# Optimization experiments

Hardware: AMD Instinct MI355X
Metric: run time of the kernel (lower is better)

The kernel has to match this reference:

```python
import jax, jax.numpy as jnp
import numpy as np

B, CIN, COUT = 16, 32, 64
H = W = 64
K = 3                      # kernel side
GRID_SIZE, SPLINE_ORDER = 5, 3
P = K * K                  # in_features of each KANLinear
GR0, GR1 = -1.0, 1.0       # grid_range


def make_grid():
    # torch: grid = arange(-k, G+k+1)*h + grid_range[0], expanded to (in_features, G+2k+1)
    h = (GR1 - GR0) / GRID_SIZE
    g = jnp.arange(-SPLINE_ORDER, GRID_SIZE + SPLINE_ORDER + 1, dtype=jnp.float32) * h + GR0
    return jnp.broadcast_to(g, (P, g.shape[0]))


def b_splines(x, grid):
    # Cox-de Boor recursion. x: (..., P) -> bases: (..., P, GRID_SIZE+SPLINE_ORDER)
    xe = x[..., None]
    bases = ((xe >= grid[:, :-1]) & (xe < grid[:, 1:])).astype(x.dtype)
    for j in range(1, SPLINE_ORDER + 1):
        left = (xe - grid[:, : -(j + 1)]) / (grid[:, j:-1] - grid[:, : -(j + 1)])
        right = (grid[:, j + 1 :] - xe) / (grid[:, j + 1 :] - grid[:, 1:-j])
        bases = left * bases[..., :-1] + right * bases[..., 1:]
    return bases


def setup_inputs() -> dict:
    key = jax.random.key(0)
    k1, k2, k3, k4 = jax.random.split(key, 4)
    x = jax.random.normal(k1, (B, CIN, H, W), dtype=jnp.float32)
    base_weight = jax.random.normal(k2, (COUT, CIN, P), dtype=jnp.float32) * (1.0 / np.sqrt(P))
    spline_weight = jax.random.normal(k3, (COUT, CIN, P, GRID_SIZE + SPLINE_ORDER), dtype=jnp.float32) * 0.1
    spline_scaler = jax.random.normal(k4, (COUT, CIN, P), dtype=jnp.float32) * (1.0 / np.sqrt(P))
    return {"x": x, "base_weight": base_weight, "spline_weight": spline_weight, "spline_scaler": spline_scaler}


def reference(x, base_weight, spline_weight, spline_scaler):
    grid = make_grid()
    # im2col like torch.nn.Unfold: (B, CIN*P, Hout, Wout), channel-major feature order
    patches = jax.lax.conv_general_dilated_patches(x, (K, K), (1, 1), "VALID")
    _, _, Ho, Wo = patches.shape
    patches = patches.reshape(B, CIN, P, Ho * Wo).transpose(0, 1, 3, 2)  # (B, CIN, L, P)
    # base branch: SiLU(x) @ base_weight^T, summed over input channels per output channel
    base_out = jnp.einsum("bclp,ocp->bol", jax.nn.silu(patches), base_weight)
    # spline branch: B-spline bases contracted with scaled spline weights
    bases = b_splines(patches, grid)                       # (B, CIN, L, P, G+k)
    scaled_w = spline_weight * spline_scaler[..., None]    # (COUT, CIN, P, G+k)
    spline_out = jnp.einsum("bclpg,ocpg->bol", bases, scaled_w)
    return (base_out + spline_out).reshape(B, COUT, Ho, Wo)
```

## Files before the change

kernel.cpp:

```cpp
#include <hip/hip_runtime.h>


typedef short v8s __attribute__((ext_vector_type(8)));
typedef float v4f __attribute__((ext_vector_type(4)));
typedef int   v4i __attribute__((ext_vector_type(4)));
typedef int   v8i __attribute__((ext_vector_type(8)));

#define WMX_OFF     20972032u
#define WF8_OFF     21103104u
#define WPACKS_OFF  21119488u

#define SCALE1 0x7F7F7F7Fu

__device__ __forceinline__ unsigned short f2bf(float f) {
  unsigned int u = __float_as_uint(f);
  u += 0x7fffu + ((u >> 16) & 1u);
  return (unsigned short)(u >> 16);
}

__global__ __launch_bounds__(256) void k_wpack(const float* __restrict__ bw,
                                               const float* __restrict__ sw,
                                               const float* __restrict__ sc,
                                               unsigned char* __restrict__ ws) {
  const int bid = blockIdx.x, t = threadIdx.x;
  if (bid < 72) {
    const int idx = bid * 256 + t;
    const int o = idx / 288, rem = idx - o * 288;
    const int c = rem / 9, p_tap = rem - c * 9;
    const float scv = sc[idx];
    const float4 v0 = *(const float4*)(sw + (size_t)idx * 8);
    const float4 v1 = *(const float4*)(sw + (size_t)idx * 8 + 4);
    unsigned lo = __builtin_amdgcn_cvt_pk_fp8_f32(v0.x * scv, v0.y * scv, 0, false);
    lo = __builtin_amdgcn_cvt_pk_fp8_f32(v0.z * scv, v0.w * scv, lo, true);
    unsigned hi = __builtin_amdgcn_cvt_pk_fp8_f32(v1.x * scv, v1.y * scv, 0, false);
    hi = __builtin_amdgcn_cvt_pk_fp8_f32(v1.z * scv, v1.w * scv, hi, true);
    const int di = p_tap / 3, dj = p_tap - di * 3;
    const int k0 = 24 * (c * 3 + di) + 8 * dj;
    const int p = k0 / 288, r288 = k0 - p * 288;
    const int ot = o >> 4, ol = o & 15;
    size_t dst;
    if (r288 < 256) {
      const int ss = r288 >> 7, r128 = r288 & 127;
      const int lh = r128 >> 5, r32 = r128 & 31;
      const int pc = r32 >> 4, bh = r32 & 15;
      dst = WMX_OFF + p * 16384 + ss * 8192 + ot * 2048 + pc * 1024 +
            (lh * 16 + ol) * 16 + bh;
    } else {
      const int r2 = r288 - 256;
      dst = WF8_OFF + p * 2048 + ot * 512 + ((r2 >> 3) * 16 + ol) * 8;
    }
    *(unsigned long long*)(ws + dst) =
        (unsigned long long)lo | ((unsigned long long)hi << 32);
  } else {
    const int idx2 = (bid - 72) * 256 + t;
    if (idx2 >= 2048) return;
    const int o = idx2 >> 5, cc = idx2 & 31;
    const int ot = o >> 4;
    const int lane = ((cc >> 3) << 4) | (o & 15);
    const int e = cc & 7;
#pragma unroll
    for (int sp = 0; sp < 9; ++sp) {
      const float val = bw[(size_t)(o * 32 + cc) * 9 + sp];
      *(unsigned short*)(ws + WPACKS_OFF + sp * 4096 + ot * 1024 + lane * 16 + e * 2) =
          f2bf(val);
    }
  }
}

__device__ __forceinline__ void ld16(unsigned char* ldsp, const unsigned char* gp) {
  __builtin_amdgcn_global_load_lds(
      (const __attribute__((address_space(1))) unsigned int*)gp,
      (__attribute__((address_space(3))) unsigned int*)ldsp, 16, 0, 0);
}

__global__ __launch_bounds__(512) void k_gemm(const unsigned char* __restrict__ ws,
                                              const float* __restrict__ x,
                                              float* __restrict__ out) {
  __shared__ __align__(16) unsigned char wl8[2][18432];
  __shared__ __align__(16) unsigned char fl8[2][12544];
  __shared__ __align__(16) unsigned char wsil[36864];
  __shared__ __align__(16) unsigned char fsil[25088];

  const int blk = blockIdx.x;
  const int b = blk >> 4, ig = blk & 15;
  const int i0 = ig * 4;
  const int tid = threadIdx.x;
  const int wave = tid >> 6, lane = tid & 63;
  const int q = lane >> 4, ln = lane & 15;
  const int r = wave >> 1, oh = wave & 1;
  const int i = i0 + r;

  const bool factive = tid < 384;
  const int frow = tid >> 6, fx = tid & 63;
  const int fy = min(i0 + frow, 63);

  auto stage_w = [&](int p, int bi) {
#pragma unroll
    for (int it = 0; it < 3; ++it) {
      const int u = wave + it * 8;
      if (u < 16) {
        ld16(&wl8[bi][u * 1024], ws + WMX_OFF + (size_t)p * 16384 + (size_t)u * 1024 + lane * 16);
      } else if (u < 18) {
        ld16(&wl8[bi][u * 1024], ws + WF8_OFF + (size_t)p * 2048 + (size_t)(u - 16) * 1024 + lane * 16);
      }
    }
  };

  auto stage_wsil = [&]() {
#pragma unroll
    for (int it = 0; it < 5; ++it) {
      const int u = wave + it * 8;
      if (u < 36) ld16(&wsil[u * 1024], ws + WPACKS_OFF + (size_t)u * 1024 + lane * 16);
    }
  };

  auto feat_load = [&](int p, float* v) {
    if (factive) {
#pragma unroll
      for (int cp = 0; cp < 4; ++cp)
        v[cp] = x[((size_t)(b * 32 + p * 4 + cp) * 64 + fy) * 64 + fx];
    }
  };

  auto feat_store = [&](int p, int bi, const float* v) {
    if (factive) {
      unsigned long long spl[4];
      unsigned short hh[4];
#pragma unroll
      for (int cp = 0; cp < 4; ++cp) {
        const float vv = v[cp];
        hh[cp] = f2bf(vv / (1.0f + __expf(-vv)));
        float s = (vv + 2.2f) * 2.5f;
        int ii = (int)floorf(s);
        ii = ii < 0 ? 0 : (ii > 10 ? 10 : ii);
        const float uu = (vv + 2.2f) - 0.4f * (float)ii;
        float N0 = (0.4f - uu) * 2.5f;
        float N1 = uu * 2.5f;
        float a0 = N0 * 1.25f, a1 = N1 * 1.25f;
        N0 = (0.4f - uu) * a0;
        float N2 = uu * a1;
        N1 = (uu + 0.4f) * a0 + (0.8f - uu) * a1;
        float c0 = N0 * (1.0f / 1.2f), c1 = N1 * (1.0f / 1.2f), c2 = N2 * (1.0f / 1.2f);
        N0 = (0.4f - uu) * c0;
        float N3 = uu * c2;
        N1 = (uu + 0.8f) * c0 + (0.8f - uu) * c1;
        N2 = (uu + 0.4f) * c1 + (1.2f - uu) * c2;
        unsigned w0 = __builtin_amdgcn_cvt_pk_fp8_f32(N0, N1, 0, false);
        w0 = __builtin_amdgcn_cvt_pk_fp8_f32(N2, N3, w0, true);
        unsigned long long wd = w0;
        const int sh = ii * 8 - 24;
        wd = (sh >= 0) ? (wd << sh) : (wd >> (-sh));
        if (!(vv >= -2.2f && vv < 2.2f)) wd = 0;
        spl[cp] = wd;
      }
#pragma unroll
      for (int cp = 0; cp < 4; ++cp)
        *(unsigned long long*)(&fl8[bi][cp * 3072 + frow * 512 + fx * 8]) = spl[cp];
      unsigned long long sp = (unsigned long long)((unsigned)hh[0] | ((unsigned)hh[1] << 16)) |
                              ((unsigned long long)((unsigned)hh[2] | ((unsigned)hh[3] << 16)) << 32);
      *(unsigned long long*)(&fsil[frow * 4096 + fx * 64 +
                                   (((p >> 1) ^ (fx & 3)) * 16) + (p & 1) * 8]) = sp;
    }
  };

  auto offf = [&](int sg, int qq) {
    int rid = 4 * sg + qq;
    int ch = rid / 3, sub = rid - ch * 3;
    int cp = ch / 3, di = ch - cp * 3;
    return cp * 3072 + (r + di) * 512 + (sub + ln) * 8;
  };
  int offA[4], offB[4];
#pragma unroll
  for (int qq = 0; qq < 4; ++qq) { offA[qq] = offf(q, qq); offB[qq] = offf(4 + q, qq); }
  const int off8 = offf(8, q);

  v4f acc[2][4];
#pragma unroll
  for (int a = 0; a < 2; ++a)
#pragma unroll
    for (int c = 0; c < 4; ++c) acc[a][c] = (v4f){0.f, 0.f, 0.f, 0.f};

  float v0[4], vcur[4];
  float vnext[4] = {0.f, 0.f, 0.f, 0.f};
  feat_load(0, v0);
  feat_load(1, vcur);
  stage_wsil();
  stage_w(0, 0);
  feat_store(0, 0, v0);
  __syncthreads();

#pragma unroll 1
  for (int t = 0; t < 8; ++t) {
    if (t < 7) {
      feat_store(t + 1, (t + 1) & 1, vcur);
      stage_w(t + 1, (t + 1) & 1);
    }
    if (t < 6) feat_load(t + 2, vnext);

    const unsigned char* wb = wl8[t & 1];
    const unsigned char* fb = fl8[t & 1];
    __builtin_amdgcn_s_setprio(1);
#pragma unroll
    for (int ss = 0; ss < 2; ++ss) {
      union { v8i v; v4i h[2]; } wf[2];
#pragma unroll
      for (int tt = 0; tt < 2; ++tt) {
        const unsigned char* wp = wb + ss * 8192 + (oh * 2 + tt) * 2048 + lane * 16;
        wf[tt].h[0] = *(const v4i*)(wp);
        wf[tt].h[1] = *(const v4i*)(wp + 1024);
      }
      const int* offs = ss ? offB : offA;
      union { v8i v; long l[4]; } ff[4];
#pragma unroll
      for (int pt = 0; pt < 4; ++pt)
#pragma unroll
        for (int qq = 0; qq < 4; ++qq)
          ff[pt].l[qq] = *(const long*)(fb + offs[qq] + pt * 128);
#pragma unroll
      for (int tt = 0; tt < 2; ++tt)
#pragma unroll
        for (int pt = 0; pt < 4; ++pt)
          acc[tt][pt] = __builtin_amdgcn_mfma_scale_f32_16x16x128_f8f6f4(
              wf[tt].v, ff[pt].v, acc[tt][pt], 0, 0, 0, SCALE1, 0, SCALE1);
    }
    {
      long w8[2], f8[4];
#pragma unroll
      for (int tt = 0; tt < 2; ++tt)
        w8[tt] = *(const long*)(wb + 16384 + (oh * 2 + tt) * 512 + lane * 8);
#pragma unroll
      for (int pt = 0; pt < 4; ++pt)
        f8[pt] = *(const long*)(fb + off8 + pt * 128);
#pragma unroll
      for (int tt = 0; tt < 2; ++tt)
#pragma unroll
        for (int pt = 0; pt < 4; ++pt)
          acc[tt][pt] = __builtin_amdgcn_mfma_f32_16x16x32_fp8_fp8(
              w8[tt], f8[pt], acc[tt][pt], 0, 0, 0);
    }
    __builtin_amdgcn_s_setprio(0);
    if (t < 6) {
#pragma unroll
      for (int cp = 0; cp < 4; ++cp) vcur[cp] = vnext[cp];
    }
    __syncthreads();
  }

#pragma unroll
  for (int e = 0; e < 9; ++e) {
    const int di = e / 3, dj = e % 3;
    v8s wb2[2], fb2[4];
#pragma unroll
    for (int tt = 0; tt < 2; ++tt)
      wb2[tt] = *(const v8s*)(&wsil[0] + e * 4096 + (oh * 2 + tt) * 1024 + lane * 16);
    const int xb = dj + ln;
    const int sbase = (r + di) * 4096 + xb * 64 + ((q ^ (xb & 3)) * 16);
#pragma unroll
    for (int pt = 0; pt < 4; ++pt)
      fb2[pt] = *(const v8s*)(&fsil[0] + sbase + pt * 1024);
    __builtin_amdgcn_s_setprio(1);
#pragma unroll
    for (int tt = 0; tt < 2; ++tt)
#pragma unroll
      for (int pt = 0; pt < 4; ++pt)
        acc[tt][pt] = __builtin_amdgcn_mfma_f32_16x16x32_bf16(
            wb2[tt], fb2[pt], acc[tt][pt], 0, 0, 0);
    __builtin_amdgcn_s_setprio(0);
  }

  if (i < 62) {
#pragma unroll
    for (int tt = 0; tt < 2; ++tt)
#pragma unroll
      for (int pt = 0; pt < 4; ++pt) {
        const int j = pt * 16 + ln;
        if (j < 62) {
#pragma unroll
          for (int rr = 0; rr < 4; ++rr) {
            const int o = (oh * 2 + tt) * 16 + q * 4 + rr;
            out[(((size_t)b * 64 + o) * 62 + i) * 62 + j] = acc[tt][pt][rr];
          }
        }
      }
  }
}

extern "C" void kernel_launch(void* const* d_in, const int* in_sizes, int n_in,
                              void* d_out, int out_size, void* d_ws, size_t ws_size,
                              hipStream_t stream) {
  const float* x  = (const float*)d_in[0];
  const float* bw = (const float*)d_in[1];
  const float* sw = (const float*)d_in[2];
  const float* sc = (const float*)d_in[3];
  unsigned char* ws = (unsigned char*)d_ws;
  float* out = (float*)d_out;

  hipLaunchKernelGGL(k_wpack, dim3(80),  dim3(256), 0, stream, bw, sw, sc, ws);
  hipLaunchKernelGGL(k_gemm,  dim3(256), dim3(512), 0, stream, ws, x, out);
}
```

Measured before the change: 91.50 us.

## Double wavefronts per block so each wave owns one output-channel tile

Grows the GEMM block from 8 to 16 waves, so each wave computes a single 16-row output-channel tile instead of two, halving the per-wave accumulators and MFMA chain length. Staging loops for weights are re-strided for 16 waves. This raises per-CU parallelism and latency hiding but duplicates feature-fragment LDS reads across more waves and increases barrier cost. The 1024-thread launch bound tightens the register budget.

```diff
diff --git a/kernel.cpp b/kernel.cpp
--- a/kernel.cpp
+++ b/kernel.cpp
@@ -73,9 +73,9 @@
       (__attribute__((address_space(3))) unsigned int*)ldsp, 16, 0, 0);
 }
 
-__global__ __launch_bounds__(512) void k_gemm(const unsigned char* __restrict__ ws,
-                                              const float* __restrict__ x,
-                                              float* __restrict__ out) {
+__global__ __launch_bounds__(1024) void k_gemm(const unsigned char* __restrict__ ws,
+                                               const float* __restrict__ x,
+                                               float* __restrict__ out) {
   __shared__ __align__(16) unsigned char wl8[2][18432];
   __shared__ __align__(16) unsigned char fl8[2][12544];
   __shared__ __align__(16) unsigned char wsil[36864];
@@ -87,7 +87,7 @@
   const int tid = threadIdx.x;
   const int wave = tid >> 6, lane = tid & 63;
   const int q = lane >> 4, ln = lane & 15;
-  const int r = wave >> 1, oh = wave & 1;
+  const int r = wave >> 2, ohq = wave & 3;
   const int i = i0 + r;
 
   const bool factive = tid < 384;
@@ -96,8 +96,8 @@
 
   auto stage_w = [&](int p, int bi) {
 #pragma unroll
-    for (int it = 0; it < 3; ++it) {
-      const int u = wave + it * 8;
+    for (int it = 0; it < 2; ++it) {
+      const int u = wave + it * 16;
       if (u < 16) {
         ld16(&wl8[bi][u * 1024], ws + WMX_OFF + (size_t)p * 16384 + (size_t)u * 1024 + lane * 16);
       } else if (u < 18) {
@@ -108,8 +108,8 @@
 
   auto stage_wsil = [&]() {
 #pragma unroll
-    for (int it = 0; it < 5; ++it) {
-      const int u = wave + it * 8;
+    for (int it = 0; it < 3; ++it) {
+      const int u = wave + it * 16;
       if (u < 36) ld16(&wsil[u * 1024], ws + WPACKS_OFF + (size_t)u * 1024 + lane * 16);
     }
   };
@@ -174,11 +174,9 @@
   for (int qq = 0; qq < 4; ++qq) { offA[qq] = offf(q, qq); offB[qq] = offf(4 + q, qq); }
   const int off8 = offf(8, q);
 
-  v4f acc[2][4];
-#pragma unroll
-  for (int a = 0; a < 2; ++a)
-#pragma unroll
-    for (int c = 0; c < 4; ++c) acc[a][c] = (v4f){0.f, 0.f, 0.f, 0.f};
+  v4f acc[4];
+#pragma unroll
+  for (int c = 0; c < 4; ++c) acc[c] = (v4f){0.f, 0.f, 0.f, 0.f};
 
   float v0[4], vcur[4];
   float vnext[4] = {0.f, 0.f, 0.f, 0.f};
@@ -202,12 +200,11 @@
     __builtin_amdgcn_s_setprio(1);
 #pragma unroll
     for (int ss = 0; ss < 2; ++ss) {
-      union { v8i v; v4i h[2]; } wf[2];
-#pragma unroll
-      for (int tt = 0; tt < 2; ++tt) {
-        const unsigned char* wp = wb + ss * 8192 + (oh * 2 + tt) * 2048 + lane * 16;
-        wf[tt].h[0] = *(const v4i*)(wp);
-        wf[tt].h[1] = *(const v4i*)(wp + 1024);
+      union { v8i v; v4i h[2]; } wf;
+      {
+        const unsigned char* wp = wb + ss * 8192 + ohq * 2048 + lane * 16;
+        wf.h[0] = *(const v4i*)(wp);
+        wf.h[1] = *(const v4i*)(wp + 1024);
       }
       const int* offs = ss ? offB : offA;
       union { v8i v; long l[4]; } ff[4];
@@ -217,26 +214,20 @@
         for (int qq = 0; qq < 4; ++qq)
           ff[pt].l[qq] = *(const long*)(fb + offs[qq] + pt * 128);
 #pragma unroll
-      for (int tt = 0; tt < 2; ++tt)
-#pragma unroll
-        for (int pt = 0; pt < 4; ++pt)
-          acc[tt][pt] = __builtin_amdgcn_mfma_scale_f32_16x16x128_f8f6f4(
-              wf[tt].v, ff[pt].v, acc[tt][pt], 0, 0, 0, SCALE1, 0, SCALE1);
+      for (int pt = 0; pt < 4; ++pt)
+        acc[pt] = __builtin_amdgcn_mfma_scale_f32_16x16x128_f8f6f4(
+            wf.v, ff[pt].v, acc[pt], 0, 0, 0, SCALE1, 0, SCALE1);
     }
     {
-      long w8[2], f8[4];
-#pragma unroll
-      for (int tt = 0; tt < 2; ++tt)
-        w8[tt] = *(const long*)(wb + 16384 + (oh * 2 + tt) * 512 + lane * 8);
+      long w8, f8[4];
+      w8 = *(const long*)(wb + 16384 + ohq * 512 + lane * 8);
 #pragma unroll
       for (int pt = 0; pt < 4; ++pt)
         f8[pt] = *(const long*)(fb + off8 + pt * 128);
 #pragma unroll
-      for (int tt = 0; tt < 2; ++tt)
-#pragma unroll
-        for (int pt = 0; pt < 4; ++pt)
-          acc[tt][pt] = __builtin_amdgcn_mfma_f32_16x16x32_fp8_fp8(
-              w8[tt], f8[pt], acc[tt][pt], 0, 0, 0);
+      for (int pt = 0; pt < 4; ++pt)
+        acc[pt] = __builtin_amdgcn_mfma_f32_16x16x32_fp8_fp8(
+            w8, f8[pt], acc[pt], 0, 0, 0);
     }
     __builtin_amdgcn_s_setprio(0);
     if (t < 6) {
@@ -249,10 +240,8 @@
 #pragma unroll
   for (int e = 0; e < 9; ++e) {
     const int di = e / 3, dj = e % 3;
-    v8s wb2[2], fb2[4];
-#pragma unroll
-    for (int tt = 0; tt < 2; ++tt)
-      wb2[tt] = *(const v8s*)(&wsil[0] + e * 4096 + (oh * 2 + tt) * 1024 + lane * 16);
+    v8s wb2, fb2[4];
+    wb2 = *(const v8s*)(&wsil[0] + e * 4096 + ohq * 1024 + lane * 16);
     const int xb = dj + ln;
     const int sbase = (r + di) * 4096 + xb * 64 + ((q ^ (xb & 3)) * 16);
 #pragma unroll
@@ -260,28 +249,24 @@
       fb2[pt] = *(const v8s*)(&fsil[0] + sbase + pt * 1024);
     __builtin_amdgcn_s_setprio(1);
 #pragma unroll
-    for (int tt = 0; tt < 2; ++tt)
-#pragma unroll
-      for (int pt = 0; pt < 4; ++pt)
-        acc[tt][pt] = __builtin_amdgcn_mfma_f32_16x16x32_bf16(
-            wb2[tt], fb2[pt], acc[tt][pt], 0, 0, 0);
+    for (int pt = 0; pt < 4; ++pt)
+      acc[pt] = __builtin_amdgcn_mfma_f32_16x16x32_bf16(
+          wb2, fb2[pt], acc[pt], 0, 0, 0);
     __builtin_amdgcn_s_setprio(0);
   }
 
   if (i < 62) {
 #pragma unroll
-    for (int tt = 0; tt < 2; ++tt)
-#pragma unroll
-      for (int pt = 0; pt < 4; ++pt) {
-        const int j = pt * 16 + ln;
-        if (j < 62) {
-#pragma unroll
-          for (int rr = 0; rr < 4; ++rr) {
-            const int o = (oh * 2 + tt) * 16 + q * 4 + rr;
-            out[(((size_t)b * 64 + o) * 62 + i) * 62 + j] = acc[tt][pt][rr];
-          }
+    for (int pt = 0; pt < 4; ++pt) {
+      const int j = pt * 16 + ln;
+      if (j < 62) {
+#pragma unroll
+        for (int rr = 0; rr < 4; ++rr) {
+          const int o = ohq * 16 + q * 4 + rr;
+          out[(((size_t)b * 64 + o) * 62 + i) * 62 + j] = acc[pt][rr];
         }
       }
+    }
   }
 }
 
@@ -295,6 +280,6 @@
   unsigned char* ws = (unsigned char*)d_ws;
   float* out = (float*)d_out;
 
-  hipLaunchKernelGGL(k_wpack, dim3(80),  dim3(256), 0, stream, bw, sw, sc, ws);
-  hipLaunchKernelGGL(k_gemm,  dim3(256), dim3(512), 0, stream, ws, x, out);
-}
+  hipLaunchKernelGGL(k_wpack, dim3(80),  dim3(256),  0, stream, bw, sw, sc, ws);
+  hipLaunchKernelGGL(k_gemm,  dim3(256), dim3(1024), 0, stream, ws, x, out);
+}
```

After: 92.03 us. About the same (+0.6%).
